# Performance work log

Measured on AMD Instinct MI355X. Metric: run time of the kernel, lower is better.

The kernel has to match this reference:

```python
import jax, jax.numpy as jnp
import numpy as np

PS = 32
EMBED_DIM = 768
IN_CH = 3
IMG = 1024
NUM_PATCHES = 992  # ini_row = i for H=1024, so need i+32 <= 1024
SPIKE_IDX = np.array([5, 300, 800])
SPIKE_VAL = 1.0e6  # makes val ~= 23.94 < 24 -> nearest size 16 -> subdivided


def _token_layout(iw_np, num_patches, ps, H):
    """Replicates the module's data-dependent patch-size / subpatch-position logic.
    Returns static (rows, cols, sizes) for every output token, in emission order."""
    avg = iw_np.mean()
    val = np.minimum(ps * avg ** 0.05 / iw_np ** 0.05, float(ps))
    choices = np.array([32, 16, 8, 4], dtype=np.float64)  # argmin picks first on tie, like min(list)
    sizes = choices[np.argmin(np.abs(val[:, None] - choices[None, :]), axis=1)].astype(np.int64)
    rows, cols, szs = [], [], []
    for i in range(num_patches):
        ini_col = (i * ps) % H
        ini_row = (i * ps * ps) // H
        s = int(sizes[i])
        if 3 < s < ps:
            ns = ps // s  # num_subpatches; subpatch_size == s
            for j in range(ns):
                rows.append(ini_row + (j * s) // ns)
                cols.append(ini_col + (j * s) % (ns * s))
                szs.append(s)
        else:
            rows.append(ini_row)
            cols.append(ini_col)
            szs.append(ps)
    return np.asarray(rows), np.asarray(cols), np.asarray(szs)


def _embed(x, W, b, rows, cols, szs, ps):
    E, C = W.shape[0], W.shape[1]
    B = x.shape[0]
    T = szs.shape[0]
    out = jnp.zeros((B, T, E), dtype=x.dtype)
    for s in np.unique(szs):
        s = int(s)
        idx = np.nonzero(szs == s)[0]  # static token slots for this size group
        r, c = rows[idx], cols[idx]
        if s == ps:
            Wf = W
        else:
            kd = ps // s  # fold the ps x ps kernel down to s x s, as in the module
            Wf = W.reshape(E, C, kd, kd, s, s).sum(axis=(2, 3))
        ar = np.arange(s)
        # gather [B, C, K, s, s] sub-patches with static advanced indexing
        patches = x[:, :, r[:, None, None] + ar[None, :, None], c[:, None, None] + ar[None, None, :]]
        tok = jnp.einsum('bckhw,echw->bke', patches, Wf) + b  # stride==kernel -> 1 token each
        out = out.at[:, jnp.asarray(idx), :].set(tok)
    return out


def setup_inputs() -> dict:
    key = jax.random.key(0)
    k_x, k_w, k_iw, k_b = jax.random.split(key, 4)
    x = jax.random.normal(k_x, (8, IN_CH, IMG, IMG), dtype=jnp.float32)
    iw = jax.random.uniform(k_iw, (1, NUM_PATCHES), dtype=jnp.float32, minval=0.5, maxval=1.5)
    iw = iw.at[0, SPIKE_IDX].set(SPIKE_VAL)  # 3 high-importance patches -> size-16 subdivision
    W = jax.random.normal(k_w, (EMBED_DIM, IN_CH, PS, PS), dtype=jnp.float32) * 0.02
    b = jax.random.normal(k_b, (EMBED_DIM,), dtype=jnp.float32) * 0.02
    return {"x": x, "importance_weights": iw, "W": W, "b": b, "num_patches": NUM_PATCHES}


def reference(x, importance_weights, W, b, num_patches):
    iw = np.asarray(importance_weights)[0]
    rows, cols, szs = _token_layout(iw, int(num_patches), PS, x.shape[3])
    return _embed(x, W, b, rows, cols, szs, PS)  # [B, T, E]
```

## Files before the change

### kernel.cpp

```cpp
#include <hip/hip_runtime.h>


typedef __attribute__((ext_vector_type(8))) short bf16x8;
typedef __attribute__((ext_vector_type(4))) float f32x4;

#define K_DIM 3072
#define N_DIM 768
#define BM 192
#define BN 128

__device__ __forceinline__ unsigned short f2bf(float f) {
  unsigned int u = __float_as_uint(f);
  u += 0x7fffu + ((u >> 16) & 1u);
  return (unsigned short)(u >> 16);
}

__device__ __forceinline__ void gload16(const void* g, void* l) {
  __builtin_amdgcn_global_load_lds(
      (const __attribute__((address_space(1))) void*)g,
      (__attribute__((address_space(3))) void*)l, 16, 0, 0);
}

__global__ __launch_bounds__(1024)
void prep_kernel(const float* __restrict__ W, unsigned short* __restrict__ Wb, int w4,
                 const float* __restrict__ iw, int P,
                 int* __restrict__ tokBase, int* __restrict__ tokMask, int NB_W) {
  int bid = blockIdx.x;
  int tid = threadIdx.x;
  if (bid < NB_W) {
    int idx = bid * 1024 + tid;
    if (idx < w4) {
      float4 f = *(const float4*)(W + (size_t)idx * 4);
      ushort4 o;
      o.x = f2bf(f.x); o.y = f2bf(f.y); o.z = f2bf(f.z); o.w = f2bf(f.w);
      *(ushort4*)(Wb + (size_t)idx * 4) = o;
    }
    return;
  }
  __shared__ double s_wsum[16];
  __shared__ double s_avg;
  __shared__ int s_cnt[1024];
  float v = (tid < P) ? iw[tid] : 0.0f;
  double d = (double)v;
#pragma unroll
  for (int off = 32; off > 0; off >>= 1) d += __shfl_down(d, off, 64);
  if ((tid & 63) == 0) s_wsum[tid >> 6] = d;
  __syncthreads();
  if (tid == 0) {
    double s = 0.0;
    for (int i = 0; i < 16; ++i) s += s_wsum[i];
    s_avg = s / (double)P;
  }
  __syncthreads();
  int cnt = 0, sz = 32;
  if (tid < P) {
    double val = 32.0 * pow(s_avg / (double)v, 0.05);
    if (val > 32.0) val = 32.0;
    sz = (val >= 24.0) ? 32 : (val >= 12.0) ? 16 : (val >= 6.0) ? 8 : 4;
    cnt = (sz < 32) ? (32 / sz) : 1;
  }
  s_cnt[tid] = cnt;
  __syncthreads();
  for (int dl = 1; dl < 1024; dl <<= 1) {
    int add = (tid >= dl) ? s_cnt[tid - dl] : 0;
    __syncthreads();
    s_cnt[tid] += add;
    __syncthreads();
  }
  if (tid < P) {
    int off = s_cnt[tid] - cnt;
    int ini_col = (tid * 32) & 1023;
    int ini_row = (tid * 32 * 32) >> 10;
    if (sz == 32) {
      tokBase[off] = ini_row * 1024 + ini_col;
      tokMask[off] = 31;
    } else {
      int ns = 32 / sz;
      for (int j = 0; j < ns; ++j) {
        int r = ini_row + (j * sz) / ns;
        int c = ini_col + ((j * sz) & 31);
        tokBase[off + j] = r * 1024 + c;
        tokMask[off + j] = sz - 1;
      }
    }
  }
}

__global__ __launch_bounds__(256)
void gather_kernel(const float* __restrict__ x,
                   const int* __restrict__ tokBase,
                   const int* __restrict__ tokMask,
                   unsigned short* __restrict__ Ab) {
  int t = blockIdx.x;
  int b = blockIdx.y;
  int T = gridDim.x;
  int m = b * T + t;
  int base = tokBase[t];
  int mask = tokMask[t];
  int sh = __popc(mask);
  const float* xb = x + (size_t)b * 3145728 + (size_t)base;
  unsigned short* arow = Ab + (size_t)m * K_DIM;
#pragma unroll
  for (int it = 0; it < 3; ++it) {
    int g = it * 256 + threadIdx.x;
    int p = g * 4;
    int c = p >> 10;
    int f = p & 1023;
    int h = (f >> sh) & mask;
    int w = f & mask;
    float4 fv = *(const float4*)(xb + (size_t)c * 1048576 + h * 1024 + w);
    ushort4 o;
    o.x = f2bf(fv.x); o.y = f2bf(fv.y); o.z = f2bf(fv.z); o.w = f2bf(fv.w);
    *(ushort4*)(arow + p) = o;
  }
}

__global__ __launch_bounds__(512)
void gemm_kernel(const unsigned short* __restrict__ A, const unsigned short* __restrict__ Wb,
                 const float* __restrict__ bias, float* __restrict__ out, int Mtot) {
  __shared__ unsigned short lds[3][20480];
  int tid = threadIdx.x;
  int lane = tid & 63;
  int wave = tid >> 6;
  int wrM = wave >> 1, wrN = wave & 1;

  int lin = blockIdx.x;
  int nwg = gridDim.x;
  int q8 = nwg >> 3, r8 = nwg & 7;
  int xcd = lin & 7, slot = lin >> 3;
  int wg = (xcd < r8) ? xcd * (q8 + 1) + slot
                      : r8 * (q8 + 1) + (xcd - r8) * q8 + slot;
  int mBase = (wg / 6) * BM;
  int nBase = (wg % 6) * BN;

  f32x4 acc[3][4] = {};

  int lrow = lane >> 3;
  int schunk = (lane & 7) ^ lrow;
  const unsigned short* Ag = A + (size_t)(mBase + wave * 24 + lrow) * K_DIM + schunk * 8;
  const unsigned short* Bg = Wb + (size_t)(nBase + wave * 16 + lrow) * K_DIM + schunk * 8;
  unsigned short* Adst0 = &lds[0][(wave * 24) * 64] + lane * 8;
  unsigned short* Bdst0 = &lds[0][12288 + (wave * 16) * 64] + lane * 8;

#define STAGE_A(BUF, KOFF)                                                  \
    _Pragma("unroll")                                                       \
    for (int inst = 0; inst < 3; ++inst)                                    \
      gload16(Ag + (size_t)(inst * 8) * K_DIM + (KOFF),                     \
              Adst0 + (size_t)(BUF) * 20480 + inst * 512);

#define STAGE_B(BUF, KOFF)                                                  \
    _Pragma("unroll")                                                       \
    for (int inst = 0; inst < 2; ++inst)                                    \
      gload16(Bg + (size_t)(inst * 8) * K_DIM + (KOFF),                     \
              Bdst0 + (size_t)(BUF) * 20480 + inst * 512);

  int rr = lane & 15, q = lane >> 4;
  int r7 = rr & 7;

#define PH(BUF, KH, STG, WAITC)                                             \
  {                                                                         \
    bf16x8 aF[3], bF[4];                                                    \
    _Pragma("unroll")                                                       \
    for (int i = 0; i < 3; ++i)                                             \
      aF[i] = *(const bf16x8*)&lds[BUF][(wrM * 48 + i * 16 + rr) * 64 +     \
                                        (((KH) * 4 + q) ^ r7) * 8];         \
    _Pragma("unroll")                                                       \
    for (int j = 0; j < 4; ++j)                                             \
      bF[j] = *(const bf16x8*)&lds[BUF][12288 +                             \
                                        (wrN * 64 + j * 16 + rr) * 64 +     \
                                        (((KH) * 4 + q) ^ r7) * 8];         \
    STG                                                                     \
    WAITC                                                                   \
    asm volatile("s_waitcnt lgkmcnt(0)" ::: "memory");                      \
    __builtin_amdgcn_s_barrier();                                           \
    __builtin_amdgcn_s_setprio(1);                                          \
    _Pragma("unroll")                                                       \
    for (int i = 0; i < 3; ++i)                                             \
      _Pragma("unroll")                                                     \
      for (int j = 0; j < 4; ++j)                                           \
        acc[i][j] = __builtin_amdgcn_mfma_f32_16x16x32_bf16(aF[i], bF[j],   \
                                                            acc[i][j], 0, 0, 0); \
    __builtin_amdgcn_s_setprio(0);                                          \
  }

#define VM5 asm volatile("s_waitcnt vmcnt(5)" ::: "memory");
#define VM0 asm volatile("s_waitcnt vmcnt(0)" ::: "memory");
#define NOP

#define ITER(BUF, SBUF, KOFF)                                               \
  PH(BUF, 0, STAGE_A(SBUF, KOFF), NOP)                                      \
  PH(BUF, 1, STAGE_B(SBUF, KOFF), VM5)

  STAGE_A(0, 0) STAGE_B(0, 0)
  STAGE_A(1, 64) STAGE_B(1, 64)
  VM5
  __builtin_amdgcn_s_barrier();

  for (int g = 0; g < 15; ++g) {
    int k = g * 192;
    ITER(0, 2, k + 128)
    ITER(1, 0, k + 192)
    ITER(2, 1, k + 256)
  }
  ITER(0, 2, 3008)
  PH(1, 0, NOP, NOP)
  PH(1, 1, NOP, VM0)
  PH(2, 0, NOP, NOP)
  PH(2, 1, NOP, NOP)
#undef ITER
#undef PH
#undef STAGE_A
#undef STAGE_B
#undef VM5
#undef VM0
#undef NOP

#pragma unroll
  for (int j = 0; j < 4; ++j) {
    int n = nBase + wrN * 64 + j * 16 + rr;
    float bv = bias[n];
#pragma unroll
    for (int i = 0; i < 3; ++i) {
      int mrow = mBase + wrM * 48 + i * 16 + q * 4;
#pragma unroll
      for (int r2 = 0; r2 < 4; ++r2) {
        int m = mrow + r2;
        if (m < Mtot) out[(size_t)m * N_DIM + n] = acc[i][j][r2] + bv;
      }
    }
  }
}

extern "C" void kernel_launch(void* const* d_in, const int* in_sizes, int n_in,
                              void* d_out, int out_size, void* d_ws, size_t ws_size,
                              hipStream_t stream) {
  const float* x  = (const float*)d_in[0];
  const float* iw = (const float*)d_in[1];
  const float* W  = (const float*)d_in[2];
  const float* b  = (const float*)d_in[3];
  int P = in_sizes[1];
  int B = in_sizes[0] / (3 * 1024 * 1024);
  int E = in_sizes[3];
  int T = out_size / (B * E);
  int Mtot = B * T;
  int mTiles = (Mtot + BM - 1) / BM;

  char* ws = (char*)d_ws;
  int* tokBase = (int*)ws;
  int* tokMask = (int*)(ws + 32768);
  unsigned short* Wb = (unsigned short*)(ws + 65536);
  unsigned short* Ab = (unsigned short*)(ws + 65536 + (size_t)E * K_DIM * 2);

  int w4 = E * K_DIM / 4;
  int NB_W = (w4 + 1023) / 1024;
  prep_kernel<<<NB_W + 1, 1024, 0, stream>>>(W, Wb, w4, iw, P, tokBase, tokMask, NB_W);

  dim3 gGrid(T, B);
  gather_kernel<<<gGrid, 256, 0, stream>>>(x, tokBase, tokMask, Ab);


  dim3 grid((N_DIM / BN) * mTiles);
  gemm_kernel<<<grid, 512, 0, stream>>>(Ab, Wb, b, (float*)d_out, Mtot);
}
```

Before: 225.3 us.

## Fuse patch gather and bf16 conversion into GEMM A-tile loading

Removes the separate gather kernel that wrote a bf16 im2col matrix to global memory. The GEMM now reads fp32 pixels directly from x via precomputed per-row base/mask tables, converts them to bf16 in registers, and stores them into LDS. The pipeline is reworked so the A loads go through registers and each phase waits on vmcnt(0). This saves the round trip of writing and re-reading the A matrix, but A loads no longer use async global-to-LDS transfers, and each A tile is re-read from x by all six N-tile workgroups, which may stall the MFMA pipeline.

```diff
diff --git a/kernel.cpp b/kernel.cpp
--- a/kernel.cpp
+++ b/kernel.cpp
@@ -15,6 +15,10 @@
   return (unsigned short)(u >> 16);
 }
 
+__device__ __forceinline__ unsigned int pk2(float a, float b) {
+  return (unsigned int)f2bf(a) | ((unsigned int)f2bf(b) << 16);
+}
+
 __device__ __forceinline__ void gload16(const void* g, void* l) {
   __builtin_amdgcn_global_load_lds(
       (const __attribute__((address_space(1))) void*)g,
@@ -24,7 +28,9 @@
 __global__ __launch_bounds__(1024)
 void prep_kernel(const float* __restrict__ W, unsigned short* __restrict__ Wb, int w4,
                  const float* __restrict__ iw, int P,
-                 int* __restrict__ tokBase, int* __restrict__ tokMask, int NB_W) {
+                 int* __restrict__ tokBase, int* __restrict__ tokMask,
+                 int* __restrict__ rowBase, int* __restrict__ rowMask,
+                 int nB, int Mpad, int NB_W) {
   int bid = blockIdx.x;
   int tid = threadIdx.x;
   if (bid < NB_W) {
@@ -84,39 +90,27 @@
       }
     }
   }
-}
-
-__global__ __launch_bounds__(256)
-void gather_kernel(const float* __restrict__ x,
-                   const int* __restrict__ tokBase,
-                   const int* __restrict__ tokMask,
-                   unsigned short* __restrict__ Ab) {
-  int t = blockIdx.x;
-  int b = blockIdx.y;
-  int T = gridDim.x;
-  int m = b * T + t;
-  int base = tokBase[t];
-  int mask = tokMask[t];
-  int sh = __popc(mask);
-  const float* xb = x + (size_t)b * 3145728 + (size_t)base;
-  unsigned short* arow = Ab + (size_t)m * K_DIM;
-#pragma unroll
-  for (int it = 0; it < 3; ++it) {
-    int g = it * 256 + threadIdx.x;
-    int p = g * 4;
-    int c = p >> 10;
-    int f = p & 1023;
-    int h = (f >> sh) & mask;
-    int w = f & mask;
-    float4 fv = *(const float4*)(xb + (size_t)c * 1048576 + h * 1024 + w);
-    ushort4 o;
-    o.x = f2bf(fv.x); o.y = f2bf(fv.y); o.z = f2bf(fv.z); o.w = f2bf(fv.w);
-    *(ushort4*)(arow + p) = o;
+  __syncthreads();
+  int Ttot = s_cnt[1023];
+  int MT = nB * Ttot;
+  for (int m = tid; m < Mpad; m += 1024) {
+    if (m < MT) {
+      int bb = m / Ttot;
+      int tt = m - bb * Ttot;
+      rowBase[m] = bb * 3145728 + tokBase[tt];
+      rowMask[m] = tokMask[tt];
+    } else {
+      rowBase[m] = 0;
+      rowMask[m] = 31;
+    }
   }
 }
 
 __global__ __launch_bounds__(512)
-void gemm_kernel(const unsigned short* __restrict__ A, const unsigned short* __restrict__ Wb,
+void gemm_kernel(const float* __restrict__ x,
+                 const int* __restrict__ rowBase,
+                 const int* __restrict__ rowMask,
+                 const unsigned short* __restrict__ Wb,
                  const float* __restrict__ bias, float* __restrict__ out, int Mtot) {
   __shared__ unsigned short lds[3][20480];
   int tid = threadIdx.x;
@@ -136,17 +130,23 @@
   f32x4 acc[3][4] = {};
 
   int lrow = lane >> 3;
+  int fo = (lane & 7) * 8;
   int schunk = (lane & 7) ^ lrow;
-  const unsigned short* Ag = A + (size_t)(mBase + wave * 24 + lrow) * K_DIM + schunk * 8;
+
   const unsigned short* Bg = Wb + (size_t)(nBase + wave * 16 + lrow) * K_DIM + schunk * 8;
-  unsigned short* Adst0 = &lds[0][(wave * 24) * 64] + lane * 8;
   unsigned short* Bdst0 = &lds[0][12288 + (wave * 16) * 64] + lane * 8;
 
-#define STAGE_A(BUF, KOFF)                                                  \
-    _Pragma("unroll")                                                       \
-    for (int inst = 0; inst < 3; ++inst)                                    \
-      gload16(Ag + (size_t)(inst * 8) * K_DIM + (KOFF),                     \
-              Adst0 + (size_t)(BUF) * 20480 + inst * 512);
+  int rbase[3], rmask[3], rsh[3];
+#pragma unroll
+  for (int i = 0; i < 3; ++i) {
+    int m = mBase + wave * 24 + i * 8 + lrow;
+    rbase[i] = rowBase[m];
+    rmask[i] = rowMask[m];
+    rsh[i]   = __popc(rmask[i]);
+  }
+  int AldsOff = (wave * 24 + lrow) * 64 + schunk * 8;
+
+  float4 aq[3][2];
 
 #define STAGE_B(BUF, KOFF)                                                  \
     _Pragma("unroll")                                                       \
@@ -154,11 +154,39 @@
       gload16(Bg + (size_t)(inst * 8) * K_DIM + (KOFF),                     \
               Bdst0 + (size_t)(BUF) * 20480 + inst * 512);
 
+#define AISSUE(KOFF)                                                        \
+  {                                                                         \
+    int f0 = ((KOFF) & 1023) + fo;                                          \
+    int c3 = (KOFF) >> 10;                                                  \
+    _Pragma("unroll")                                                       \
+    for (int i = 0; i < 3; ++i) {                                           \
+      int h0 = (f0 >> rsh[i]) & rmask[i];                                   \
+      int w0 = f0 & rmask[i];                                               \
+      int h1 = ((f0 + 4) >> rsh[i]) & rmask[i];                             \
+      int w1 = (f0 + 4) & rmask[i];                                         \
+      const float* p = x + (size_t)(rbase[i] + (c3 << 20));                 \
+      aq[i][0] = *(const float4*)(p + (h0 << 10) + w0);                     \
+      aq[i][1] = *(const float4*)(p + (h1 << 10) + w1);                     \
+    }                                                                       \
+  }
+
+#define ACONV(BUF)                                                          \
+  {                                                                         \
+    _Pragma("unroll")                                                       \
+    for (int i = 0; i < 3; ++i) {                                           \
+      uint4 v;                                                              \
+      v.x = pk2(aq[i][0].x, aq[i][0].y);                                    \
+      v.y = pk2(aq[i][0].z, aq[i][0].w);                                    \
+      v.z = pk2(aq[i][1].x, aq[i][1].y);                                    \
+      v.w = pk2(aq[i][1].z, aq[i][1].w);                                    \
+      *(uint4*)&lds[BUF][AldsOff + i * 512] = v;                            \
+    }                                                                       \
+  }
+
   int rr = lane & 15, q = lane >> 4;
   int r7 = rr & 7;
 
-#define PH(BUF, KH, STG, WAITC)                                             \
-  {                                                                         \
+#define FRAGS(BUF, KH)                                                      \
     bf16x8 aF[3], bF[4];                                                    \
     _Pragma("unroll")                                                       \
     for (int i = 0; i < 3; ++i)                                             \
@@ -168,9 +196,9 @@
     for (int j = 0; j < 4; ++j)                                             \
       bF[j] = *(const bf16x8*)&lds[BUF][12288 +                             \
                                         (wrN * 64 + j * 16 + rr) * 64 +     \
-                                        (((KH) * 4 + q) ^ r7) * 8];         \
-    STG                                                                     \
-    WAITC                                                                   \
+                                        (((KH) * 4 + q) ^ r7) * 8];
+
+#define MF                                                                  \
     asm volatile("s_waitcnt lgkmcnt(0)" ::: "memory");                      \
     __builtin_amdgcn_s_barrier();                                           \
     __builtin_amdgcn_s_setprio(1);                                          \
@@ -180,40 +208,42 @@
       for (int j = 0; j < 4; ++j)                                           \
         acc[i][j] = __builtin_amdgcn_mfma_f32_16x16x32_bf16(aF[i], bF[j],   \
                                                             acc[i][j], 0, 0, 0); \
-    __builtin_amdgcn_s_setprio(0);                                          \
-  }
-
-#define VM5 asm volatile("s_waitcnt vmcnt(5)" ::: "memory");
-#define VM0 asm volatile("s_waitcnt vmcnt(0)" ::: "memory");
-#define NOP
-
-#define ITER(BUF, SBUF, KOFF)                                               \
-  PH(BUF, 0, STAGE_A(SBUF, KOFF), NOP)                                      \
-  PH(BUF, 1, STAGE_B(SBUF, KOFF), VM5)
-
-  STAGE_A(0, 0) STAGE_B(0, 0)
-  STAGE_A(1, 64) STAGE_B(1, 64)
-  VM5
+    __builtin_amdgcn_s_setprio(0);
+
+#define PH0(BUF, SBUF, KOFF) { FRAGS(BUF, 0) STAGE_B(SBUF, KOFF) AISSUE(KOFF) MF }
+#define PH1(BUF, SBUF)                                                      \
+  { FRAGS(BUF, 1) ACONV(SBUF)                                               \
+    asm volatile("s_waitcnt vmcnt(0)" ::: "memory"); MF }
+#define PH0N(BUF) { FRAGS(BUF, 0) MF }
+#define PH1N(BUF) { FRAGS(BUF, 1) MF }
+#define ITER(BUF, SBUF, KOFF) PH0(BUF, SBUF, KOFF) PH1(BUF, SBUF)
+
+  STAGE_B(0, 0)
+  AISSUE(0)
+  ACONV(0)
+  asm volatile("s_waitcnt vmcnt(0)" ::: "memory");
+  asm volatile("s_waitcnt lgkmcnt(0)" ::: "memory");
   __builtin_amdgcn_s_barrier();
 
   for (int g = 0; g < 15; ++g) {
     int k = g * 192;
-    ITER(0, 2, k + 128)
-    ITER(1, 0, k + 192)
-    ITER(2, 1, k + 256)
-  }
-  ITER(0, 2, 3008)
-  PH(1, 0, NOP, NOP)
-  PH(1, 1, NOP, VM0)
-  PH(2, 0, NOP, NOP)
-  PH(2, 1, NOP, NOP)
+    ITER(0, 1, k + 64)
+    ITER(1, 2, k + 128)
+    ITER(2, 0, k + 192)
+  }
+  ITER(0, 1, 2944)
+  ITER(1, 2, 3008)
+  PH0N(2) PH1N(2)
 #undef ITER
-#undef PH
-#undef STAGE_A
+#undef PH0
+#undef PH1
+#undef PH0N
+#undef PH1N
+#undef MF
+#undef FRAGS
+#undef ACONV
+#undef AISSUE
 #undef STAGE_B
-#undef VM5
-#undef VM0
-#undef NOP
 
 #pragma unroll
   for (int j = 0; j < 4; ++j) {
@@ -244,21 +274,21 @@
   int T = out_size / (B * E);
   int Mtot = B * T;
   int mTiles = (Mtot + BM - 1) / BM;
+  int Mpad = mTiles * BM;
 
   char* ws = (char*)d_ws;
   int* tokBase = (int*)ws;
   int* tokMask = (int*)(ws + 32768);
-  unsigned short* Wb = (unsigned short*)(ws + 65536);
-  unsigned short* Ab = (unsigned short*)(ws + 65536 + (size_t)E * K_DIM * 2);
+  int* rowBase = (int*)(ws + 65536);
+  int* rowMask = (int*)(ws + 98304);
+  unsigned short* Wb = (unsigned short*)(ws + 131072);
 
   int w4 = E * K_DIM / 4;
   int NB_W = (w4 + 1023) / 1024;
-  prep_kernel<<<NB_W + 1, 1024, 0, stream>>>(W, Wb, w4, iw, P, tokBase, tokMask, NB_W);
-
-  dim3 gGrid(T, B);
-  gather_kernel<<<gGrid, 256, 0, stream>>>(x, tokBase, tokMask, Ab);
-
+  prep_kernel<<<NB_W + 1, 1024, 0, stream>>>(W, Wb, w4, iw, P, tokBase, tokMask,
+                                             rowBase, rowMask, B, Mpad, NB_W);
 
   dim3 grid((N_DIM / BN) * mTiles);
-  gemm_kernel<<<grid, 512, 0, stream>>>(Ab, Wb, b, (float*)d_out, Mtot);
-}
+  gemm_kernel<<<grid, 512, 0, stream>>>(x, rowBase, rowMask, Wb, b,
+                                        (float*)d_out, Mtot);
+}
```

Measured after the change: 259.3 us. 1.15x slower.

## Split GEMM K dimension in two with atomic accumulation and double buffering

Applied to the files above, without the earlier changes.

The GEMM grid is doubled so each workgroup handles half of the K dimension, and partial sums go into a pre-zeroed output through float atomic adds. The bias is added only by the first half. The LDS pipeline drops from triple to double buffering with a full vmcnt(0) wait each iteration, and the XCD-aware mapping is replaced by a hardcoded (lin&7)*63 mapping. This adds a memset and atomic traffic and assumes the grid size is exactly 504 workgroups.

```diff
diff --git a/kernel.cpp b/kernel.cpp
--- a/kernel.cpp
+++ b/kernel.cpp
@@ -118,20 +118,19 @@
 __global__ __launch_bounds__(512)
 void gemm_kernel(const unsigned short* __restrict__ A, const unsigned short* __restrict__ Wb,
                  const float* __restrict__ bias, float* __restrict__ out, int Mtot) {
-  __shared__ unsigned short lds[3][20480];
+  __shared__ unsigned short lds[2][20480];
   int tid = threadIdx.x;
   int lane = tid & 63;
   int wave = tid >> 6;
   int wrM = wave >> 1, wrN = wave & 1;
 
   int lin = blockIdx.x;
-  int nwg = gridDim.x;
-  int q8 = nwg >> 3, r8 = nwg & 7;
-  int xcd = lin & 7, slot = lin >> 3;
-  int wg = (xcd < r8) ? xcd * (q8 + 1) + slot
-                      : r8 * (q8 + 1) + (xcd - r8) * q8 + slot;
-  int mBase = (wg / 6) * BM;
-  int nBase = (wg % 6) * BN;
+  int wg = (lin & 7) * 63 + (lin >> 3);
+  int mBase = (wg / 12) * BM;
+  int rem = wg % 12;
+  int khalf = rem / 6;
+  int nBase = (rem % 6) * BN;
+  int kStart = khalf * (K_DIM / 2);
 
   f32x4 acc[3][4] = {};
 
@@ -183,49 +182,44 @@
     __builtin_amdgcn_s_setprio(0);                                          \
   }
 
-#define VM5 asm volatile("s_waitcnt vmcnt(5)" ::: "memory");
 #define VM0 asm volatile("s_waitcnt vmcnt(0)" ::: "memory");
 #define NOP
 
-#define ITER(BUF, SBUF, KOFF)                                               \
-  PH(BUF, 0, STAGE_A(SBUF, KOFF), NOP)                                      \
-  PH(BUF, 1, STAGE_B(SBUF, KOFF), VM5)
-
-  STAGE_A(0, 0) STAGE_B(0, 0)
-  STAGE_A(1, 64) STAGE_B(1, 64)
-  VM5
+#define ITER(BUF, KOFF)                                                     \
+  PH(BUF, 0, STAGE_A(BUF ^ 1, KOFF) STAGE_B(BUF ^ 1, KOFF), NOP)            \
+  PH(BUF, 1, NOP, VM0)
+
+  STAGE_A(0, kStart) STAGE_B(0, kStart)
+  VM0
   __builtin_amdgcn_s_barrier();
 
-  for (int g = 0; g < 15; ++g) {
-    int k = g * 192;
-    ITER(0, 2, k + 128)
-    ITER(1, 0, k + 192)
-    ITER(2, 1, k + 256)
-  }
-  ITER(0, 2, 3008)
+  for (int g = 0; g < 11; ++g) {
+    int k = kStart + g * 128;
+    ITER(0, k + 64)
+    ITER(1, k + 128)
+  }
+  ITER(0, kStart + 1472)
   PH(1, 0, NOP, NOP)
-  PH(1, 1, NOP, VM0)
-  PH(2, 0, NOP, NOP)
-  PH(2, 1, NOP, NOP)
+  PH(1, 1, NOP, NOP)
 #undef ITER
 #undef PH
 #undef STAGE_A
 #undef STAGE_B
-#undef VM5
 #undef VM0
 #undef NOP
 
 #pragma unroll
   for (int j = 0; j < 4; ++j) {
     int n = nBase + wrN * 64 + j * 16 + rr;
-    float bv = bias[n];
+    float bv = (khalf == 0) ? bias[n] : 0.0f;
 #pragma unroll
     for (int i = 0; i < 3; ++i) {
       int mrow = mBase + wrM * 48 + i * 16 + q * 4;
 #pragma unroll
       for (int r2 = 0; r2 < 4; ++r2) {
         int m = mrow + r2;
-        if (m < Mtot) out[(size_t)m * N_DIM + n] = acc[i][j][r2] + bv;
+        if (m < Mtot) unsafeAtomicAdd(&out[(size_t)m * N_DIM + n],
+                                      acc[i][j][r2] + bv);
       }
     }
   }
@@ -251,6 +245,8 @@
   unsigned short* Wb = (unsigned short*)(ws + 65536);
   unsigned short* Ab = (unsigned short*)(ws + 65536 + (size_t)E * K_DIM * 2);
 
+  hipMemsetAsync(d_out, 0, (size_t)out_size * sizeof(float), stream);
+
   int w4 = E * K_DIM / 4;
   int NB_W = (w4 + 1023) / 1024;
   prep_kernel<<<NB_W + 1, 1024, 0, stream>>>(W, Wb, w4, iw, P, tokBase, tokMask, NB_W);
@@ -259,6 +255,6 @@
   gather_kernel<<<gGrid, 256, 0, stream>>>(x, tokBase, tokMask, Ab);
 
 
-  dim3 grid((N_DIM / BN) * mTiles);
+  dim3 grid((N_DIM / BN) * mTiles * 2);
   gemm_kernel<<<grid, 512, 0, stream>>>(Ab, Wb, b, (float*)d_out, Mtot);
 }
```

Result: slower. 259.3 us (+15.1%).
